# Kernel optimization log

Hardware: AMD Instinct MI355X
Metric: run time of the kernel (lower is better)

## Reference

```python
import jax, jax.numpy as jnp
import numpy as np

B, DIM = 64, 1024

def setup_inputs() -> dict:
    key = jax.random.key(0)
    ks = jax.random.split(key, 16)
    d = {
        'x': jax.random.normal(ks[0], (B, DIM), jnp.float32),
        'C': jax.random.normal(ks[1], (B, DIM, DIM), jnp.float32) * 0.02,
        'n': jax.random.normal(ks[2], (B, DIM), jnp.float32),
        'm': jax.random.normal(ks[3], (B, DIM), jnp.float32),
    }
    s = 1.0 / np.sqrt(DIM)
    names = ['q', 'k', 'v', 'i', 'f', 'o']
    for j, nm in enumerate(names):
        d['W' + nm] = jax.random.uniform(ks[4 + 2 * j], (DIM, DIM), jnp.float32, -s, s)
        d['b' + nm] = jax.random.uniform(ks[5 + 2 * j], (DIM,), jnp.float32, -s, s)
    return d

def _lin(x, W, b):
    # torch nn.Linear: x @ W.T + b
    return x @ W.T + b

def reference(x, C, n, m, Wq, bq, Wk, bk, Wv, bv, Wi, bi, Wf, bf, Wo, bo):
    q = _lin(x, Wq, bq)                      # [B, D]
    k = _lin(x, Wk, bk) / jnp.sqrt(jnp.float32(DIM))
    v = _lin(x, Wv, bv)
    i_t = _lin(x, Wi, bi)
    f_t = _lin(x, Wf, bf)
    m_new = jnp.maximum(f_t + m, i_t)        # [B, D]
    i = jnp.exp(i_t - m_new)                 # [B, D]
    f = jnp.exp(f_t + m - m_new)             # [B, D]
    # rank-1 covariance update: C_new[b,r,c] = f[b,r]*C[b,r,c] + i[b,r]*v[b,r]*k[b,c]
    C_new = f[:, :, None] * C + (i * v)[:, :, None] * k[:, None, :]
    n_new = f * n + i * k
    h = jax.nn.sigmoid(_lin(x, Wo, bo)) * jnp.einsum('brc,bc->br', C_new, q)
    return (h, C_new, n_new, m_new)
```

## Files before the change

### kernel.cpp

```cpp
#include <hip/hip_runtime.h>
#include <math.h>

#define BATCH 64
#define DIM 1024
#define NROW (BATCH * DIM)
#define OFF_H 0
#define OFF_C 65536
#define OFF_N (65536 + 67108864)
#define OFF_M (OFF_N + 65536)


__global__ __launch_bounds__(256) void gemm6(
    const float* __restrict__ x,
    const float* __restrict__ Wq, const float* __restrict__ bq,
    const float* __restrict__ Wk, const float* __restrict__ bk,
    const float* __restrict__ Wv, const float* __restrict__ bv,
    const float* __restrict__ Wi, const float* __restrict__ bi,
    const float* __restrict__ Wf, const float* __restrict__ bf,
    const float* __restrict__ Wo, const float* __restrict__ bo,
    float* __restrict__ pre)
{
    __shared__ float xs[64][64];
    __shared__ float wl[64][17];

    const int bx = blockIdx.x;
    const int g = bx >> 6;
    const int j0 = (bx & 63) * 16;
    const float* W; const float* bias;
    switch (g) {
        case 0: W = Wq; bias = bq; break;
        case 1: W = Wk; bias = bk; break;
        case 2: W = Wv; bias = bv; break;
        case 3: W = Wi; bias = bi; break;
        case 4: W = Wf; bias = bf; break;
        default: W = Wo; bias = bo; break;
    }

    const int tid = threadIdx.x;
    const int tj = tid & 15;
    const int tb = tid >> 4;

    const int xb = tid & 63;
    const int xc = tid >> 6;
    const int wj = tid >> 4;
    const int wk = tid & 15;

    float acc[4] = {0.f, 0.f, 0.f, 0.f};

    for (int k0 = 0; k0 < DIM; k0 += 64) {
        #pragma unroll
        for (int it = 0; it < 4; ++it) {
            const int cq = xc * 4 + it;
            float4 v = *reinterpret_cast<const float4*>(&x[xb * DIM + k0 + cq * 4]);
            xs[cq * 4 + 0][xb] = v.x;
            xs[cq * 4 + 1][xb] = v.y;
            xs[cq * 4 + 2][xb] = v.z;
            xs[cq * 4 + 3][xb] = v.w;
        }
        {
            float4 v = *reinterpret_cast<const float4*>(&W[(j0 + wj) * DIM + k0 + wk * 4]);
            wl[wk * 4 + 0][wj] = v.x;
            wl[wk * 4 + 1][wj] = v.y;
            wl[wk * 4 + 2][wj] = v.z;
            wl[wk * 4 + 3][wj] = v.w;
        }
        __syncthreads();
        #pragma unroll
        for (int kk = 0; kk < 64; ++kk) {
            float4 xv = *reinterpret_cast<const float4*>(&xs[kk][tb * 4]);
            float wv = wl[kk][tj];
            acc[0] += xv.x * wv;
            acc[1] += xv.y * wv;
            acc[2] += xv.z * wv;
            acc[3] += xv.w * wv;
        }
        __syncthreads();
    }

    const float bv_ = bias[j0 + tj];
    const int jcol = j0 + tj;
    #pragma unroll
    for (int e = 0; e < 4; ++e) {
        const int b = tb * 4 + e;
        pre[g * NROW + b * DIM + jcol] = acc[e] + bv_;
    }
}

__global__ __launch_bounds__(256) void derive(
    const float* __restrict__ n_in, const float* __restrict__ m_in,
    float* __restrict__ ws, float* __restrict__ out)
{
    const int idx = blockIdx.x * 256 + threadIdx.x;
    const float kp  = ws[1 * NROW + idx];
    const float vp  = ws[2 * NROW + idx];
    const float ip  = ws[3 * NROW + idx];
    const float fp_ = ws[4 * NROW + idx];
    const float op  = ws[5 * NROW + idx];
    const float mo = m_in[idx];
    const float no = n_in[idx];

    const float ks  = kp * 0.03125f;
    const float mn  = fmaxf(fp_ + mo, ip);
    const float iex = expf(ip - mn);
    const float fex = expf(fp_ + mo - mn);
    const float so  = 1.f / (1.f + expf(-op));

    ws[1 * NROW + idx] = ks;
    ws[2 * NROW + idx] = iex * vp;
    ws[4 * NROW + idx] = fex;
    ws[5 * NROW + idx] = so;
    out[OFF_N + idx] = fex * no + iex * ks;
    out[OFF_M + idx] = mn;
}

__global__ __launch_bounds__(256) void cupdate(
    const float* __restrict__ C,
    const float* __restrict__ ws,
    float* __restrict__ out)
{
    const int row  = blockIdx.x * 4 + (threadIdx.x >> 6);
    const int lane = threadIdx.x & 63;
    const int b    = row >> 10;

    const float f_r = ws[4 * NROW + row];
    const float iv  = ws[2 * NROW + row];
    const float so  = ws[5 * NROW + row];

    const float4* k4 = reinterpret_cast<const float4*>(ws + 1 * NROW + b * DIM);
    const float4* q4 = reinterpret_cast<const float4*>(ws + 0 * NROW + b * DIM);
    const float4* C4 = reinterpret_cast<const float4*>(C) + (size_t)row * 256;
    float4*       O4 = reinterpret_cast<float4*>(out + OFF_C) + (size_t)row * 256;

    float dot = 0.f;
    #pragma unroll
    for (int i = 0; i < 4; ++i) {
        const int c4 = lane + 64 * i;
        float4 cv = C4[c4];
        float4 kv = k4[c4];
        float4 qv = q4[c4];
        float4 cn;
        cn.x = f_r * cv.x + iv * kv.x;
        cn.y = f_r * cv.y + iv * kv.y;
        cn.z = f_r * cv.z + iv * kv.z;
        cn.w = f_r * cv.w + iv * kv.w;
        O4[c4] = cn;
        dot += cn.x * qv.x + cn.y * qv.y + cn.z * qv.z + cn.w * qv.w;
    }
    #pragma unroll
    for (int off = 32; off > 0; off >>= 1)
        dot += __shfl_xor(dot, off, 64);
    if (lane == 0)
        out[OFF_H + row] = so * dot;
}

extern "C" void kernel_launch(void* const* d_in, const int* in_sizes, int n_in,
                              void* d_out, int out_size, void* d_ws, size_t ws_size,
                              hipStream_t stream) {
    const float* x = (const float*)d_in[0];
    const float* C = (const float*)d_in[1];
    const float* n = (const float*)d_in[2];
    const float* m = (const float*)d_in[3];
    float* ws  = (float*)d_ws;
    float* out = (float*)d_out;

    gemm6<<<384, 256, 0, stream>>>(
        x,
        (const float*)d_in[4],  (const float*)d_in[5],
        (const float*)d_in[6],  (const float*)d_in[7],
        (const float*)d_in[8],  (const float*)d_in[9],
        (const float*)d_in[10], (const float*)d_in[11],
        (const float*)d_in[12], (const float*)d_in[13],
        (const float*)d_in[14], (const float*)d_in[15],
        ws);
    derive<<<NROW / 256, 256, 0, stream>>>(n, m, ws, out);
    cupdate<<<NROW / 4, 256, 0, stream>>>(C, ws, out);
}
```

Measured before the change: 139.4 us.

## Fuse gate derivation into C update kernel and use nontemporal C loads/stores

Removes the separate derive kernel. Each cupdate wave now computes m_new, the exp gates, the sigmoid and n_new for its own row, and applies the 1/sqrt(D) scale to k inside the update through a folded scalar. C is streamed with nontemporal loads and stores so it does not pollute the cache. This saves one launch and one round trip through the workspace, at the cost of redundant per-row scalar exp work inside each wave.

```diff
diff --git a/kernel.cpp b/kernel.cpp
--- a/kernel.cpp
+++ b/kernel.cpp
@@ -8,6 +8,8 @@
 #define OFF_C 65536
 #define OFF_N (65536 + 67108864)
 #define OFF_M (OFF_N + 65536)
+
+typedef float f4 __attribute__((ext_vector_type(4)));
 
 
 __global__ __launch_bounds__(256) void gemm6(
@@ -86,35 +88,9 @@
     }
 }
 
-__global__ __launch_bounds__(256) void derive(
-    const float* __restrict__ n_in, const float* __restrict__ m_in,
-    float* __restrict__ ws, float* __restrict__ out)
-{
-    const int idx = blockIdx.x * 256 + threadIdx.x;
-    const float kp  = ws[1 * NROW + idx];
-    const float vp  = ws[2 * NROW + idx];
-    const float ip  = ws[3 * NROW + idx];
-    const float fp_ = ws[4 * NROW + idx];
-    const float op  = ws[5 * NROW + idx];
-    const float mo = m_in[idx];
-    const float no = n_in[idx];
-
-    const float ks  = kp * 0.03125f;
-    const float mn  = fmaxf(fp_ + mo, ip);
-    const float iex = expf(ip - mn);
-    const float fex = expf(fp_ + mo - mn);
-    const float so  = 1.f / (1.f + expf(-op));
-
-    ws[1 * NROW + idx] = ks;
-    ws[2 * NROW + idx] = iex * vp;
-    ws[4 * NROW + idx] = fex;
-    ws[5 * NROW + idx] = so;
-    out[OFF_N + idx] = fex * no + iex * ks;
-    out[OFF_M + idx] = mn;
-}
-
 __global__ __launch_bounds__(256) void cupdate(
     const float* __restrict__ C,
+    const float* __restrict__ n_in, const float* __restrict__ m_in,
     const float* __restrict__ ws,
     float* __restrict__ out)
 {
@@ -122,35 +98,48 @@
     const int lane = threadIdx.x & 63;
     const int b    = row >> 10;
 
-    const float f_r = ws[4 * NROW + row];
-    const float iv  = ws[2 * NROW + row];
-    const float so  = ws[5 * NROW + row];
+    const float ip  = ws[3 * NROW + row];
+    const float fp_ = ws[4 * NROW + row];
+    const float op  = ws[5 * NROW + row];
+    const float vp  = ws[2 * NROW + row];
+    const float mo  = m_in[row];
 
-    const float4* k4 = reinterpret_cast<const float4*>(ws + 1 * NROW + b * DIM);
-    const float4* q4 = reinterpret_cast<const float4*>(ws + 0 * NROW + b * DIM);
-    const float4* C4 = reinterpret_cast<const float4*>(C) + (size_t)row * 256;
-    float4*       O4 = reinterpret_cast<float4*>(out + OFF_C) + (size_t)row * 256;
+    const float mn  = fmaxf(fp_ + mo, ip);
+    const float iex = expf(ip - mn);
+    const float fex = expf(fp_ + mo - mn);
+    const float so  = 1.f / (1.f + expf(-op));
+    const float iv  = iex * vp;
+
+    const f4* k4 = reinterpret_cast<const f4*>(ws + 1 * NROW + b * DIM);
+    const f4* q4 = reinterpret_cast<const f4*>(ws + 0 * NROW + b * DIM);
+    const f4* C4 = reinterpret_cast<const f4*>(C) + (size_t)row * 256;
+    f4*       O4 = reinterpret_cast<f4*>(out + OFF_C) + (size_t)row * 256;
+
+    const float ksc = iv * 0.03125f;
 
     float dot = 0.f;
     #pragma unroll
     for (int i = 0; i < 4; ++i) {
         const int c4 = lane + 64 * i;
-        float4 cv = C4[c4];
-        float4 kv = k4[c4];
-        float4 qv = q4[c4];
-        float4 cn;
-        cn.x = f_r * cv.x + iv * kv.x;
-        cn.y = f_r * cv.y + iv * kv.y;
-        cn.z = f_r * cv.z + iv * kv.z;
-        cn.w = f_r * cv.w + iv * kv.w;
-        O4[c4] = cn;
-        dot += cn.x * qv.x + cn.y * qv.y + cn.z * qv.z + cn.w * qv.w;
+        f4 cv = __builtin_nontemporal_load(&C4[c4]);
+        f4 kv = k4[c4];
+        f4 qv = q4[c4];
+        f4 cn = fex * cv + ksc * kv;
+        __builtin_nontemporal_store(cn, &O4[c4]);
+        f4 pr = cn * qv;
+        dot += pr.x + pr.y + pr.z + pr.w;
     }
     #pragma unroll
     for (int off = 32; off > 0; off >>= 1)
         dot += __shfl_xor(dot, off, 64);
-    if (lane == 0)
+
+    if (lane == 0) {
         out[OFF_H + row] = so * dot;
+        const float no   = n_in[row];
+        const float kp_r = ws[1 * NROW + row] * 0.03125f;
+        out[OFF_N + row] = fex * no + iex * kp_r;
+        out[OFF_M + row] = mn;
+    }
 }
 
 extern "C" void kernel_launch(void* const* d_in, const int* in_sizes, int n_in,
@@ -172,6 +161,5 @@
         (const float*)d_in[12], (const float*)d_in[13],
         (const float*)d_in[14], (const float*)d_in[15],
         ws);
-    derive<<<NROW / 256, 256, 0, stream>>>(n, m, ws, out);
-    cupdate<<<NROW / 4, 256, 0, stream>>>(C, ws, out);
+    cupdate<<<NROW / 4, 256, 0, stream>>>(C, n, m, ws, out);
 }
```

Result: faster. 135.6 us (-2.7%).
